# Kernel tuning notes

Measured on AMD Instinct MI355X. Metric: run time of the kernel, lower is better.

The kernel has to match this reference:

```python
import jax, jax.numpy as jnp
import numpy as np

EPS = 1e-5          # calc_mean_std eps
C = 256             # feature channels
N_PER = 32          # patches per side-group
SIDES = (24, 32, 48)
OUT = 56            # AdaptiveAvgPool2d target


def _pool_matrix(s, o=OUT):
    """Exact torch AdaptiveAvgPool2d as a [o, s] averaging matrix."""
    P = np.zeros((o, s), np.float32)
    for i in range(o):
        start = (i * s) // o
        end = -((-(i + 1) * s) // o)  # ceil((i+1)*s/o)
        P[i, start:end] = 1.0 / (end - start)
    return jnp.asarray(P)

_POOL = {s: _pool_matrix(s) for s in SIDES}


def setup_inputs() -> dict:
    key = jax.random.key(0)
    ks = jax.random.split(key, len(SIDES))
    out = {}
    means, stds = [], []
    for k, s in zip(ks, SIDES):
        raw = jax.random.normal(k, (N_PER, C, s, s), dtype=jnp.float32)
        # calc_mean_std: per (patch, channel) spatial mean / unbiased std
        m = raw.mean(axis=(2, 3), keepdims=True)
        v = raw.var(axis=(2, 3), keepdims=True, ddof=1)
        sd = jnp.sqrt(v + EPS)
        out[f"patches_{s}"] = (raw - m) / sd  # pre-normalized, as in __init__
        means.append(m)
        stds.append(sd)
    out["style_mean"] = jnp.concatenate(means, axis=0)  # [96, C, 1, 1]
    out["style_std"] = jnp.concatenate(stds, axis=0)    # [96, C, 1, 1]
    return out


def _denorm_relu_pool(x, mean, std, P):
    # x: [n, C, s, s]; affine denorm + ReLU + adaptive avg pool to 56x56
    t = jax.nn.relu(x * std + mean)
    y = jnp.einsum('oi,ncij->ncoj', P, t)   # pool rows
    y = jnp.einsum('ncoj,pj->ncop', y, P)   # pool cols
    return y


def reference(patches_24, patches_32, patches_48, style_mean, style_std):
    groups = ((patches_24, 24, 0), (patches_32, 32, N_PER), (patches_48, 48, 2 * N_PER))
    outs = []
    for x, s, lo in groups:
        n = x.shape[0]
        outs.append(_denorm_relu_pool(x, style_mean[lo:lo + n], style_std[lo:lo + n], _POOL[s]))
    return jnp.concatenate(outs, axis=0)  # [96, C, 56, 56]
```

## Files before the change

kernel.cpp:

```cpp
#include <hip/hip_runtime.h>


#define C_CH 256
#define OUTS 56
#define NPER 32

template<int S>
__device__ __forceinline__ void group_body(const float* __restrict__ x,
                                           const float* __restrict__ smean,
                                           const float* __restrict__ sstd,
                                           float* __restrict__ out,
                                           int local_bid, int n_base,
                                           float* __restrict__ lds) {
    const int n_local = local_bid >> 8;
    const int c       = local_bid & 255;
    const int n_glob  = n_base + n_local;
    const float mn = smean[n_glob * C_CH + c];
    const float sd = sstd [n_glob * C_CH + c];

    const float* xin = x + (size_t)(n_local * C_CH + c) * (S * S);
    const int tid = threadIdx.x;

    constexpr int NV = (S * S) / 4;
    const float4* x4 = (const float4*)xin;
    float4* l4 = (float4*)lds;
    for (int idx = tid; idx < NV; idx += 256) {
        float4 v = x4[idx];
        v.x = fmaxf(fmaf(v.x, sd, mn), 0.0f);
        v.y = fmaxf(fmaf(v.y, sd, mn), 0.0f);
        v.z = fmaxf(fmaf(v.z, sd, mn), 0.0f);
        v.w = fmaxf(fmaf(v.w, sd, mn), 0.0f);
        l4[idx] = v;
    }
    __syncthreads();

    float* outp = out + (size_t)(n_glob * C_CH + c) * (OUTS * OUTS);
    float4* out4 = (float4*)outp;

    constexpr int NQ = (OUTS * OUTS) / 4;
    for (int q = tid; q < NQ; q += 256) {
        const int i  = q / (OUTS / 4);
        const int j0 = (q % (OUTS / 4)) * 4;
        const int r0 = (i * S) / OUTS;
        const int r1 = ((i + 1) * S + OUTS - 1) / OUTS;
        const int rc = r1 - r0;

        float o[4];
        #pragma unroll
        for (int k = 0; k < 4; ++k) {
            const int j  = j0 + k;
            const int c0 = (j * S) / OUTS;
            const int c1 = ((j + 1) * S + OUTS - 1) / OUTS;
            const int cc = c1 - c0;
            float acc = lds[r0 * S + c0];
            if (cc == 2) acc += lds[r0 * S + c0 + 1];
            if (rc == 2) {
                acc += lds[(r0 + 1) * S + c0];
                if (cc == 2) acc += lds[(r0 + 1) * S + c0 + 1];
            }
            o[k] = acc * (1.0f / (float)(rc * cc));
        }
        float4 v; v.x = o[0]; v.y = o[1]; v.z = o[2]; v.w = o[3];
        out4[q] = v;
    }
}

__global__ __launch_bounds__(256) void PPIN_DC_20753281974843_kernel(
        const float* __restrict__ p24, const float* __restrict__ p32,
        const float* __restrict__ p48, const float* __restrict__ smean,
        const float* __restrict__ sstd, float* __restrict__ out) {
    __shared__ float lds[48 * 48];
    const int bid   = blockIdx.x;
    const int group = bid >> 13;
    const int local = bid & 8191;
    if (group == 0)      group_body<24>(p24, smean, sstd, out, local, 0,        lds);
    else if (group == 1) group_body<32>(p32, smean, sstd, out, local, NPER,     lds);
    else                 group_body<48>(p48, smean, sstd, out, local, 2 * NPER, lds);
}

extern "C" void kernel_launch(void* const* d_in, const int* in_sizes, int n_in,
                              void* d_out, int out_size, void* d_ws, size_t ws_size,
                              hipStream_t stream) {
    const float* p24   = (const float*)d_in[0];
    const float* p32   = (const float*)d_in[1];
    const float* p48   = (const float*)d_in[2];
    const float* smean = (const float*)d_in[3];
    const float* sstd  = (const float*)d_in[4];
    float* out = (float*)d_out;

    PPIN_DC_20753281974843_kernel<<<dim3(24576), dim3(256), 0, stream>>>(
        p24, p32, p48, smean, sstd, out);
}
```

Baseline: 392.9 us.

## Process four maps per block with double-buffered LDS prefetch and nontemporal stores

Each block now handles four consecutive (patch, channel) maps instead of one. The next map's input is loaded into registers while the current map is pooled from one of two LDS buffers, which overlaps global loads with pooling and output writes. Output stores become nontemporal, and the reciprocal divide is replaced by 0.5/1.0 selects. The aim is to hide load latency and cut per-block overhead in this write-bound kernel, at the cost of fewer blocks (less parallelism) and twice the LDS.

New measurement: 414.2 us. +5.4%, slower.

```diff
diff --git a/kernel.cpp b/kernel.cpp
--- a/kernel.cpp
+++ b/kernel.cpp
@@ -4,47 +4,24 @@
 #define C_CH 256
 #define OUTS 56
 #define NPER 32
+#define MPB  4
+#define BPG  ((NPER * C_CH) / MPB)
+
+typedef float f4 __attribute__((ext_vector_type(4)));
 
 template<int S>
-__device__ __forceinline__ void group_body(const float* __restrict__ x,
-                                           const float* __restrict__ smean,
-                                           const float* __restrict__ sstd,
-                                           float* __restrict__ out,
-                                           int local_bid, int n_base,
-                                           float* __restrict__ lds) {
-    const int n_local = local_bid >> 8;
-    const int c       = local_bid & 255;
-    const int n_glob  = n_base + n_local;
-    const float mn = smean[n_glob * C_CH + c];
-    const float sd = sstd [n_glob * C_CH + c];
-
-    const float* xin = x + (size_t)(n_local * C_CH + c) * (S * S);
+__device__ __forceinline__ void compute_map(const float* __restrict__ buf,
+                                            float* __restrict__ outp) {
     const int tid = threadIdx.x;
-
-    constexpr int NV = (S * S) / 4;
-    const float4* x4 = (const float4*)xin;
-    float4* l4 = (float4*)lds;
-    for (int idx = tid; idx < NV; idx += 256) {
-        float4 v = x4[idx];
-        v.x = fmaxf(fmaf(v.x, sd, mn), 0.0f);
-        v.y = fmaxf(fmaf(v.y, sd, mn), 0.0f);
-        v.z = fmaxf(fmaf(v.z, sd, mn), 0.0f);
-        v.w = fmaxf(fmaf(v.w, sd, mn), 0.0f);
-        l4[idx] = v;
-    }
-    __syncthreads();
-
-    float* outp = out + (size_t)(n_glob * C_CH + c) * (OUTS * OUTS);
-    float4* out4 = (float4*)outp;
-
     constexpr int NQ = (OUTS * OUTS) / 4;
+    f4* __restrict__ out4 = (f4*)outp;
     for (int q = tid; q < NQ; q += 256) {
         const int i  = q / (OUTS / 4);
         const int j0 = (q % (OUTS / 4)) * 4;
         const int r0 = (i * S) / OUTS;
         const int r1 = ((i + 1) * S + OUTS - 1) / OUTS;
         const int rc = r1 - r0;
-
+        const float invr = (rc == 2) ? 0.5f : 1.0f;
         float o[4];
         #pragma unroll
         for (int k = 0; k < 4; ++k) {
@@ -52,16 +29,93 @@
             const int c0 = (j * S) / OUTS;
             const int c1 = ((j + 1) * S + OUTS - 1) / OUTS;
             const int cc = c1 - c0;
-            float acc = lds[r0 * S + c0];
-            if (cc == 2) acc += lds[r0 * S + c0 + 1];
+            float acc = buf[r0 * S + c0];
+            if (cc == 2) acc += buf[r0 * S + c0 + 1];
             if (rc == 2) {
-                acc += lds[(r0 + 1) * S + c0];
-                if (cc == 2) acc += lds[(r0 + 1) * S + c0 + 1];
+                acc += buf[(r0 + 1) * S + c0];
+                if (cc == 2) acc += buf[(r0 + 1) * S + c0 + 1];
             }
-            o[k] = acc * (1.0f / (float)(rc * cc));
+            const float invc = (cc == 2) ? 0.5f : 1.0f;
+            o[k] = acc * invr * invc;
         }
-        float4 v; v.x = o[0]; v.y = o[1]; v.z = o[2]; v.w = o[3];
-        out4[q] = v;
+        f4 v;
+        v.x = o[0]; v.y = o[1]; v.z = o[2]; v.w = o[3];
+        __builtin_nontemporal_store(v, &out4[q]);
+    }
+}
+
+template<int S>
+__device__ __forceinline__ void group_body(const float* __restrict__ x,
+                                           const float* __restrict__ smean,
+                                           const float* __restrict__ sstd,
+                                           float* __restrict__ out,
+                                           int lb, int n_base,
+                                           float* __restrict__ lds) {
+    constexpr int NV  = (S * S) / 4;
+    constexpr int RPT = (NV + 255) / 256;
+    const int tid = threadIdx.x;
+    const int m0  = lb * MPB;
+
+    float mns[MPB], sds[MPB];
+    #pragma unroll
+    for (int t = 0; t < MPB; ++t) {
+        mns[t] = smean[(size_t)n_base * C_CH + m0 + t];
+        sds[t] = sstd [(size_t)n_base * C_CH + m0 + t];
+    }
+
+    float* __restrict__ b0 = lds;
+    float* __restrict__ b1 = lds + S * S;
+    const f4* __restrict__ xall = (const f4*)x;
+
+    f4 pref[RPT];
+
+    #pragma unroll
+    for (int u = 0; u < RPT; ++u) {
+        const int idx = tid + u * 256;
+        if (idx < NV) pref[u] = xall[(size_t)m0 * NV + idx];
+    }
+    #pragma unroll
+    for (int u = 0; u < RPT; ++u) {
+        const int idx = tid + u * 256;
+        if (idx < NV) {
+            f4 v = pref[u];
+            v.x = fmaxf(fmaf(v.x, sds[0], mns[0]), 0.0f);
+            v.y = fmaxf(fmaf(v.y, sds[0], mns[0]), 0.0f);
+            v.z = fmaxf(fmaf(v.z, sds[0], mns[0]), 0.0f);
+            v.w = fmaxf(fmaf(v.w, sds[0], mns[0]), 0.0f);
+            ((f4*)b0)[idx] = v;
+        }
+    }
+    __syncthreads();
+
+    #pragma unroll
+    for (int t = 0; t < MPB; ++t) {
+        float* const cur = (t & 1) ? b1 : b0;
+        float* const nxt = (t & 1) ? b0 : b1;
+        if (t + 1 < MPB) {
+            #pragma unroll
+            for (int u = 0; u < RPT; ++u) {
+                const int idx = tid + u * 256;
+                if (idx < NV) pref[u] = xall[(size_t)(m0 + t + 1) * NV + idx];
+            }
+        }
+        compute_map<S>(cur,
+            out + (size_t)((size_t)n_base * C_CH + m0 + t) * (OUTS * OUTS));
+        if (t + 1 < MPB) {
+            #pragma unroll
+            for (int u = 0; u < RPT; ++u) {
+                const int idx = tid + u * 256;
+                if (idx < NV) {
+                    f4 v = pref[u];
+                    v.x = fmaxf(fmaf(v.x, sds[t + 1], mns[t + 1]), 0.0f);
+                    v.y = fmaxf(fmaf(v.y, sds[t + 1], mns[t + 1]), 0.0f);
+                    v.z = fmaxf(fmaf(v.z, sds[t + 1], mns[t + 1]), 0.0f);
+                    v.w = fmaxf(fmaf(v.w, sds[t + 1], mns[t + 1]), 0.0f);
+                    ((f4*)nxt)[idx] = v;
+                }
+            }
+        }
+        __syncthreads();
     }
 }
 
@@ -69,13 +123,13 @@
         const float* __restrict__ p24, const float* __restrict__ p32,
         const float* __restrict__ p48, const float* __restrict__ smean,
         const float* __restrict__ sstd, float* __restrict__ out) {
-    __shared__ float lds[48 * 48];
+    __shared__ float lds[2 * 48 * 48];
     const int bid   = blockIdx.x;
-    const int group = bid >> 13;
-    const int local = bid & 8191;
-    if (group == 0)      group_body<24>(p24, smean, sstd, out, local, 0,        lds);
-    else if (group == 1) group_body<32>(p32, smean, sstd, out, local, NPER,     lds);
-    else                 group_body<48>(p48, smean, sstd, out, local, 2 * NPER, lds);
+    const int group = bid >> 11;
+    const int lb    = bid & (BPG - 1);
+    if (group == 0)      group_body<24>(p24, smean, sstd, out, lb, 0,        lds);
+    else if (group == 1) group_body<32>(p32, smean, sstd, out, lb, NPER,     lds);
+    else                 group_body<48>(p48, smean, sstd, out, lb, 2 * NPER, lds);
 }
 
 extern "C" void kernel_launch(void* const* d_in, const int* in_sizes, int n_in,
@@ -88,6 +142,6 @@
     const float* sstd  = (const float*)d_in[4];
     float* out = (float*)d_out;
 
-    PPIN_DC_20753281974843_kernel<<<dim3(24576), dim3(256), 0, stream>>>(
+    PPIN_DC_20753281974843_kernel<<<dim3(3 * BPG), dim3(256), 0, stream>>>(
         p24, p32, p48, smean, sstd, out);
 }
```

## Drop LDS staging; gather and denormalize inputs directly from global memory

Applied to the files above, without the earlier changes.

Removes the shared-memory tile and the block-wide barrier. Each output thread now loads its up-to-4 source pixels straight from global memory (served by L1/L2) and applies the denorm+ReLU per load. This removes the LDS round-trip and the sync, which should help occupancy and latency. The cost is redundant, uncoalesced scalar global loads and repeated FMA work for overlapping pixels, and it relies on cache hits for reuse.

Result: slower. 531.9 us (+35.4%).

```diff
diff --git a/kernel.cpp b/kernel.cpp
--- a/kernel.cpp
+++ b/kernel.cpp
@@ -5,45 +5,33 @@
 #define OUTS 56
 #define NPER 32
 
+typedef float f4 __attribute__((ext_vector_type(4)));
+
 template<int S>
 __device__ __forceinline__ void group_body(const float* __restrict__ x,
                                            const float* __restrict__ smean,
                                            const float* __restrict__ sstd,
                                            float* __restrict__ out,
-                                           int local_bid, int n_base,
-                                           float* __restrict__ lds) {
+                                           int local_bid, int n_base) {
     const int n_local = local_bid >> 8;
     const int c       = local_bid & 255;
     const int n_glob  = n_base + n_local;
     const float mn = smean[n_glob * C_CH + c];
     const float sd = sstd [n_glob * C_CH + c];
 
-    const float* xin = x + (size_t)(n_local * C_CH + c) * (S * S);
-    const int tid = threadIdx.x;
-
-    constexpr int NV = (S * S) / 4;
-    const float4* x4 = (const float4*)xin;
-    float4* l4 = (float4*)lds;
-    for (int idx = tid; idx < NV; idx += 256) {
-        float4 v = x4[idx];
-        v.x = fmaxf(fmaf(v.x, sd, mn), 0.0f);
-        v.y = fmaxf(fmaf(v.y, sd, mn), 0.0f);
-        v.z = fmaxf(fmaf(v.z, sd, mn), 0.0f);
-        v.w = fmaxf(fmaf(v.w, sd, mn), 0.0f);
-        l4[idx] = v;
-    }
-    __syncthreads();
-
-    float* outp = out + (size_t)(n_glob * C_CH + c) * (OUTS * OUTS);
-    float4* out4 = (float4*)outp;
+    const float* __restrict__ xin = x + (size_t)(n_local * C_CH + c) * (S * S);
+    f4* __restrict__ out4 = (f4*)(out + (size_t)(n_glob * C_CH + c) * (OUTS * OUTS));
 
     constexpr int NQ = (OUTS * OUTS) / 4;
-    for (int q = tid; q < NQ; q += 256) {
+    for (int q = threadIdx.x; q < NQ; q += 256) {
         const int i  = q / (OUTS / 4);
         const int j0 = (q % (OUTS / 4)) * 4;
         const int r0 = (i * S) / OUTS;
         const int r1 = ((i + 1) * S + OUTS - 1) / OUTS;
-        const int rc = r1 - r0;
+        const int rtwo = r1 - r0 - 1;
+        const float invr = rtwo ? 0.5f : 1.0f;
+        const float* __restrict__ row0 = xin + r0 * S;
+        const float* __restrict__ row1 = row0 + rtwo * S;
 
         float o[4];
         #pragma unroll
@@ -51,16 +39,25 @@
             const int j  = j0 + k;
             const int c0 = (j * S) / OUTS;
             const int c1 = ((j + 1) * S + OUTS - 1) / OUTS;
-            const int cc = c1 - c0;
-            float acc = lds[r0 * S + c0];
-            if (cc == 2) acc += lds[r0 * S + c0 + 1];
-            if (rc == 2) {
-                acc += lds[(r0 + 1) * S + c0];
-                if (cc == 2) acc += lds[(r0 + 1) * S + c0 + 1];
+            const int ctwo = c1 - c0 - 1;
+            float a00 = row0[c0];
+            float a01 = row0[c0 + ctwo];
+            float a10 = row1[c0];
+            float a11 = row1[c0 + ctwo];
+            a00 = fmaxf(fmaf(a00, sd, mn), 0.0f);
+            a01 = fmaxf(fmaf(a01, sd, mn), 0.0f);
+            a10 = fmaxf(fmaf(a10, sd, mn), 0.0f);
+            a11 = fmaxf(fmaf(a11, sd, mn), 0.0f);
+            float acc = a00;
+            if (ctwo) acc += a01;
+            if (rtwo) {
+                acc += a10;
+                if (ctwo) acc += a11;
             }
-            o[k] = acc * (1.0f / (float)(rc * cc));
+            const float invc = ctwo ? 0.5f : 1.0f;
+            o[k] = acc * (invr * invc);
         }
-        float4 v; v.x = o[0]; v.y = o[1]; v.z = o[2]; v.w = o[3];
+        f4 v; v.x = o[0]; v.y = o[1]; v.z = o[2]; v.w = o[3];
         out4[q] = v;
     }
 }
@@ -69,13 +66,12 @@
         const float* __restrict__ p24, const float* __restrict__ p32,
         const float* __restrict__ p48, const float* __restrict__ smean,
         const float* __restrict__ sstd, float* __restrict__ out) {
-    __shared__ float lds[48 * 48];
     const int bid   = blockIdx.x;
     const int group = bid >> 13;
     const int local = bid & 8191;
-    if (group == 0)      group_body<24>(p24, smean, sstd, out, local, 0,        lds);
-    else if (group == 1) group_body<32>(p32, smean, sstd, out, local, NPER,     lds);
-    else                 group_body<48>(p48, smean, sstd, out, local, 2 * NPER, lds);
+    if (group == 0)      group_body<24>(p24, smean, sstd, out, local, 0);
+    else if (group == 1) group_body<32>(p32, smean, sstd, out, local, NPER);
+    else                 group_body<48>(p48, smean, sstd, out, local, 2 * NPER);
 }
 
 extern "C" void kernel_launch(void* const* d_in, const int* in_sizes, int n_in,
```
